# Optimization experiments

Measured on AMD Instinct MI355X. Metric: run time of the kernel, lower is better.

The kernel has to match this reference:

```python
import jax, jax.numpy as jnp
import numpy as np

B, T, C, H = 2, 2048, 1024, 16
D = C // H  # head dim


def setup_inputs() -> dict:
    key = jax.random.key(0)
    k1, k2, k3 = jax.random.split(key, 3)
    x = jax.random.normal(k1, (B, T, C), dtype=jnp.float32)
    w_qkv = jax.random.normal(k2, (3 * C, C), dtype=jnp.float32) * (1.0 / np.sqrt(C))
    b_qkv = jnp.zeros((3 * C,), dtype=jnp.float32)
    w_proj = jax.random.normal(k3, (C, C), dtype=jnp.float32) * (1.0 / np.sqrt(C))
    b_proj = jnp.zeros((C,), dtype=jnp.float32)
    return {"x": x, "w_qkv": w_qkv, "b_qkv": b_qkv, "w_proj": w_proj, "b_proj": b_proj}


def reference(x, w_qkv, b_qkv, w_proj, b_proj):
    # torch Linear: y = x @ W^T + b
    qkv = jnp.einsum('btc,oc->bto', x, w_qkv) + b_qkv  # [B,T,3C]
    q, k, v = jnp.split(qkv, 3, axis=-1)
    # [B,T,C] -> [B,H,T,D]
    reshape = lambda t: t.reshape(B, T, H, D).transpose(0, 2, 1, 3)
    q, k, v = reshape(q), reshape(k), reshape(v)
    scale = 1.0 / jnp.sqrt(jnp.float32(C))  # NOTE: full C, as in source
    att = jnp.einsum('bhtd,bhsd->bhts', q, k) * scale  # [B,H,T,T]
    causal = jnp.tril(jnp.ones((T, T), dtype=bool))
    att = jnp.where(causal, att, -jnp.inf)
    att = jax.nn.softmax(att, axis=-1)
    y = jnp.einsum('bhts,bhsd->bhtd', att, v)  # [B,H,T,D]
    y = y.transpose(0, 2, 1, 3).reshape(B, T, C)
    return jnp.einsum('btc,oc->bto', y, w_proj) + b_proj
```

## Files before the change

### kernel.cpp

```cpp
#include <hip/hip_runtime.h>

#define DEVINL __device__ __forceinline__

typedef __attribute__((ext_vector_type(8))) short short8;
typedef __attribute__((ext_vector_type(4))) float f32x4;

DEVINL unsigned f2bf_u(float x) {
  union { float f; unsigned u; } v; v.f = x;
  unsigned r = v.u + 0x7FFF + ((v.u >> 16) & 1);
  return r >> 16;
}
DEVINL unsigned short f2bf(float x) { return (unsigned short)f2bf_u(x); }

DEVINL unsigned cvt_pk_bf16(float lo, float hi) {
  unsigned r;
  asm("v_cvt_pk_bf16_f32 %0, %1, %2" : "=v"(r) : "v"(lo), "v"(hi));
  return r;
}

DEVINL void permlane32_swap(unsigned& a, unsigned& b) {
  asm volatile("v_permlane32_swap_b32 %0, %1" : "+v"(a), "+v"(b));
}
DEVINL void permlane16_swap(unsigned& a, unsigned& b) {
  asm volatile("v_permlane16_swap_b32 %0, %1" : "+v"(a), "+v"(b));
}

#if __has_builtin(__builtin_amdgcn_exp2f)
#define EXP2(x) __builtin_amdgcn_exp2f(x)
#else
#define EXP2(x) exp2f(x)
#endif

DEVINL void gload_lds16(const void* g, void* l) {
  __builtin_amdgcn_global_load_lds(
      (const __attribute__((address_space(1))) unsigned int*)g,
      (__attribute__((address_space(3))) unsigned int*)l, 16, 0, 0);
}

DEVINL short8 as_s8(uint4 v) { union { uint4 u; short8 s; } c; c.u = v; return c.s; }
DEVINL f32x4 fzero() { f32x4 z = {0.f, 0.f, 0.f, 0.f}; return z; }

__global__ __launch_bounds__(256) void cvt3_kernel(
    const float4* __restrict__ x, const float4* __restrict__ wq,
    const float4* __restrict__ wp, ushort4* __restrict__ xo,
    ushort4* __restrict__ wqo, ushort4* __restrict__ wpo) {
  const int N1 = 1048576, N2 = 1835008, NT = 2097152;
  int i = blockIdx.x * blockDim.x + threadIdx.x;
  int stride = gridDim.x * blockDim.x;
  for (; i < NT; i += stride) {
    const float4* s; ushort4* d; int j;
    if (i < N1) { s = x; d = xo; j = i; }
    else if (i < N2) { s = wq; d = wqo; j = i - N1; }
    else { s = wp; d = wpo; j = i - N2; }
    float4 v = s[j];
    ushort4 o;
    o.x = f2bf(v.x); o.y = f2bf(v.y); o.z = f2bf(v.z); o.w = f2bf(v.w);
    d[j] = o;
  }
}

template <int RX, int RY>
__global__ __launch_bounds__(256, 2) void gemm_qkv(
    const ushort* __restrict__ A, const ushort* __restrict__ Bw,
    const float* __restrict__ bias,
    ushort* __restrict__ Qb, ushort* __restrict__ Kb, ushort* __restrict__ Vt,
    int M, int N, int K) {
  __shared__ __align__(16) char smem[32768];
  char* ldsA = smem;
  char* ldsB = smem + 16384;

  int gx = gridDim.x;
  int id = blockIdx.y * gx + blockIdx.x;
  int xcd = id & 7, slot = id >> 3;
  int rw = gx / RX, rh = gridDim.y / RY;
  int bx = (xcd % RX) * rw + slot % rw;
  int by = (xcd / RX) * rh + slot / rw;

  int m0 = by * 128, n0 = bx * 128;
  int t = threadIdx.x;
  int lane = t & 63, w = t >> 6;
  int q = lane & 15, g = lane >> 4;
  int wr = w >> 1, wc = w & 1;

  int Lrow[4], Lcol[4];
#pragma unroll
  for (int i = 0; i < 4; ++i) {
    int L = i * 4096 + t * 16;
    int row = L >> 7, c = L & 127;
    Lrow[i] = row;
    Lcol[i] = c ^ ((row & 7) << 4);
  }
  const char* Abase = (const char*)A + (size_t)m0 * K * 2;
  const char* Bbase = (const char*)Bw + (size_t)n0 * K * 2;

  f32x4 acc[4][4];
#pragma unroll
  for (int i = 0; i < 4; ++i)
#pragma unroll
    for (int j = 0; j < 4; ++j) acc[i][j] = fzero();

  for (int k0 = 0; k0 < K; k0 += 64) {
    __syncthreads();
#pragma unroll
    for (int i = 0; i < 4; ++i) {
      int L = i * 4096 + t * 16;
      gload_lds16(Abase + (size_t)Lrow[i] * (K * 2) + k0 * 2 + Lcol[i], ldsA + L);
    }
#pragma unroll
    for (int i = 0; i < 4; ++i) {
      int L = i * 4096 + t * 16;
      gload_lds16(Bbase + (size_t)Lrow[i] * (K * 2) + k0 * 2 + Lcol[i], ldsB + L);
    }
    __syncthreads();

    uint4 bf[2][4];
#pragma unroll
    for (int s = 0; s < 2; ++s)
#pragma unroll
      for (int nt = 0; nt < 4; ++nt) {
        int row = wc * 64 + nt * 16 + q;
        int addr = row * 128 + ((g * 16 + 64 * s) ^ ((row & 7) << 4));
        bf[s][nt] = *(const uint4*)(ldsB + addr);
      }
#pragma unroll
    for (int mt = 0; mt < 4; ++mt) {
      int row = wr * 64 + mt * 16 + q;
      int a0 = row * 128 + ((g * 16) ^ ((row & 7) << 4));
      int a1 = row * 128 + ((g * 16 + 64) ^ ((row & 7) << 4));
      uint4 af0 = *(const uint4*)(ldsA + a0);
      uint4 af1 = *(const uint4*)(ldsA + a1);
#pragma unroll
      for (int nt = 0; nt < 4; ++nt) {
        acc[mt][nt] = __builtin_amdgcn_mfma_f32_16x16x32_bf16(
            as_s8(af0), as_s8(bf[0][nt]), acc[mt][nt], 0, 0, 0);
        acc[mt][nt] = __builtin_amdgcn_mfma_f32_16x16x32_bf16(
            as_s8(af1), as_s8(bf[1][nt]), acc[mt][nt], 0, 0, 0);
      }
    }
  }

  int mrow0 = m0 + wr * 64;
  int b = mrow0 >> 11, tt0 = mrow0 & 2047;
  if (n0 >= 2048) {
    int hs = (n0 + wc * 64) >> 6;
    int h = hs & 15;
    ushort* vb = Vt + ((size_t)(b * 16 + h) * 64) * 2048;
#pragma unroll
    for (int nt = 0; nt < 4; ++nt) {
      int d = nt * 16 + q;
      float bv = bias[n0 + wc * 64 + nt * 16 + q];
#pragma unroll
      for (int mt = 0; mt < 4; ++mt) {
        uint2 o;
        o.x = cvt_pk_bf16(acc[mt][nt][0] + bv, acc[mt][nt][1] + bv);
        o.y = cvt_pk_bf16(acc[mt][nt][2] + bv, acc[mt][nt][3] + bv);
        *(uint2*)(vb + (size_t)d * 2048 + tt0 + mt * 16 + g * 4) = o;
      }
    }
  } else {
    __syncthreads();
    char* tile = smem + w * 8192;
    float bv[4];
#pragma unroll
    for (int nt = 0; nt < 4; ++nt) bv[nt] = bias[n0 + wc * 64 + nt * 16 + q];
#pragma unroll
    for (int mt = 0; mt < 4; ++mt)
#pragma unroll
      for (int nt = 0; nt < 4; ++nt)
#pragma unroll
        for (int r = 0; r < 4; ++r) {
          int row = mt * 16 + g * 4 + r;
          int bcol = ((nt * 16 + q) * 2) ^ ((row & 7) << 4);
          *(ushort*)(tile + row * 128 + bcol) = f2bf(acc[mt][nt][r] + bv[nt]);
        }
    int hs = (n0 + wc * 64) >> 6;
    int which = hs >> 4, h = hs & 15;
    ushort* dst = which == 0 ? Qb : Kb;
    ushort* dbase = dst + (size_t)(b * 16 + h) * 131072 + (size_t)tt0 * 64;
#pragma unroll
    for (int p = 0; p < 8; ++p) {
      int row = p * 8 + (lane >> 3);
      int bcol = ((lane & 7) * 16) ^ ((row & 7) << 4);
      uint4 v = *(const uint4*)(tile + row * 128 + bcol);
      *(uint4*)(dbase + (size_t)row * 64 + (lane & 7) * 8) = v;
    }
  }
}

__global__ __launch_bounds__(256, 2) void gemm_proj(
    const ushort* __restrict__ A, const ushort* __restrict__ Bw,
    const float* __restrict__ bias, float* __restrict__ Out,
    int M, int N, int K) {
  __shared__ __align__(16) char smem[24576];

  int gx = gridDim.x;
  int id = blockIdx.y * gx + blockIdx.x;
  int xcd = id & 7, slot = id >> 3;
  int bx = slot & 7;
  int by = xcd * 8 + (slot >> 3);

  int m0 = by * 64, n0 = bx * 128;
  int t = threadIdx.x;
  int lane = t & 63, w = t >> 6;
  int q = lane & 15, g = lane >> 4;
  int wr = w >> 1, wc = w & 1;

  int Lrow[4], Lcol[4];
#pragma unroll
  for (int i = 0; i < 4; ++i) {
    int L = i * 4096 + t * 16;
    int row = L >> 7, c = L & 127;
    Lrow[i] = row;
    Lcol[i] = c ^ ((row & 7) << 4);
  }
  const char* Abase = (const char*)A + (size_t)m0 * K * 2;
  const char* Bbase = (const char*)Bw + (size_t)n0 * K * 2;

  f32x4 acc[2][4];
#pragma unroll
  for (int i = 0; i < 2; ++i)
#pragma unroll
    for (int j = 0; j < 4; ++j) acc[i][j] = fzero();

  for (int k0 = 0; k0 < K; k0 += 64) {
    __syncthreads();
#pragma unroll
    for (int i = 0; i < 2; ++i) {
      int L = i * 4096 + t * 16;
      gload_lds16(Abase + (size_t)Lrow[i] * (K * 2) + k0 * 2 + Lcol[i], smem + L);
    }
#pragma unroll
    for (int i = 0; i < 4; ++i) {
      int L = i * 4096 + t * 16;
      gload_lds16(Bbase + (size_t)Lrow[i] * (K * 2) + k0 * 2 + Lcol[i],
                  smem + 8192 + L);
    }
    __syncthreads();

    uint4 bf[2][4];
#pragma unroll
    for (int s = 0; s < 2; ++s)
#pragma unroll
      for (int nt = 0; nt < 4; ++nt) {
        int row = wc * 64 + nt * 16 + q;
        int addr = 8192 + row * 128 + ((g * 16 + 64 * s) ^ ((row & 7) << 4));
        bf[s][nt] = *(const uint4*)(smem + addr);
      }
    __builtin_amdgcn_s_setprio(1);
#pragma unroll
    for (int mt = 0; mt < 2; ++mt) {
      int row = wr * 32 + mt * 16 + q;
      int a0 = row * 128 + ((g * 16) ^ ((row & 7) << 4));
      int a1 = row * 128 + ((g * 16 + 64) ^ ((row & 7) << 4));
      uint4 af0 = *(const uint4*)(smem + a0);
      uint4 af1 = *(const uint4*)(smem + a1);
#pragma unroll
      for (int nt = 0; nt < 4; ++nt) {
        acc[mt][nt] = __builtin_amdgcn_mfma_f32_16x16x32_bf16(
            as_s8(af0), as_s8(bf[0][nt]), acc[mt][nt], 0, 0, 0);
        acc[mt][nt] = __builtin_amdgcn_mfma_f32_16x16x32_bf16(
            as_s8(af1), as_s8(bf[1][nt]), acc[mt][nt], 0, 0, 0);
      }
    }
    __builtin_amdgcn_s_setprio(0);
  }

#pragma unroll
  for (int nt = 0; nt < 4; ++nt) {
    int ncol = n0 + wc * 64 + nt * 16 + q;
    float bv = bias[ncol];
#pragma unroll
    for (int mt = 0; mt < 2; ++mt)
#pragma unroll
      for (int r = 0; r < 4; ++r) {
        int m = m0 + wr * 32 + mt * 16 + g * 4 + r;
        Out[(size_t)m * N + ncol] = acc[mt][nt][r] + bv;
      }
  }
}

__global__ __launch_bounds__(512) void attn_kernel(
    const ushort* __restrict__ Q, const ushort* __restrict__ K,
    const ushort* __restrict__ Vt, ushort* __restrict__ Y) {
  __shared__ __align__(16) char smem[33280];
  const float C44 = 0.0450842298f;
  int id = blockIdx.x;
  int xcd = id & 7, slot = id >> 3;
  int bh = xcd * 4 + (slot & 3);
  int qt = 31 - (slot >> 2);
  int t = threadIdx.x;
  int lane = t & 63, w = t >> 6;
  int q = lane & 15, g = lane >> 4;
  int wq = w & 3, half = w >> 2;
  int b = bh >> 4, hh = bh & 15;

  const char* Kc0 = (const char*)(K + (size_t)bh * 2048 * 64);
  const char* Vc0 = (const char*)(Vt + (size_t)bh * 64 * 2048);

  int tb = t * 16;
  int srow = tb >> 7;
  int scol = (tb & 127) ^ ((srow & 7) << 4);

  int offK[2][2], offV[4];
#pragma unroll
  for (int sub = 0; sub < 2; ++sub)
#pragma unroll
    for (int s = 0; s < 2; ++s) {
      int row = half * 32 + sub * 16 + q;
      offK[sub][s] = row * 128 + ((g * 16 + 64 * s) ^ ((row & 7) << 4));
    }
#pragma unroll
  for (int ds = 0; ds < 4; ++ds) {
    int row = ds * 16 + q;
    offV[ds] = 8192 + row * 128 + ((half * 64 + g * 16) ^ ((row & 7) << 4));
  }

  int nch = qt + 1;
  int qrow0 = qt * 64 + wq * 16;
  int qg = qrow0 + q;

  uint4 qf[2];
  {
    const ushort* Qrow = Q + ((size_t)bh * 2048 + qrow0 + q) * 64;
    qf[0] = *(const uint4*)(Qrow + g * 8);
    qf[1] = *(const uint4*)(Qrow + 32 + g * 8);
  }

  f32x4 oacc[4];
#pragma unroll
  for (int i = 0; i < 4; ++i) oacc[i] = fzero();
  float l_run = 0.f;

  gload_lds16(Kc0 + (size_t)srow * 128 + scol, smem + tb);
  gload_lds16(Vc0 + (size_t)srow * 4096 + scol, smem + 8192 + tb);
  __syncthreads();

  int cur = 0;
#pragma unroll 1
  for (int c = 0; c < nch; ++c) {
    int kv0 = c * 64;
    if (c + 1 < nch) {
      int kn = kv0 + 64;
      char* dstb = smem + (cur ^ 1) * 16384;
      gload_lds16(Kc0 + (size_t)(kn + srow) * 128 + scol, dstb + tb);
      gload_lds16(Vc0 + (size_t)srow * 4096 + (size_t)kn * 2 + scol,
                  dstb + 8192 + tb);
    }
    const char* base = smem + cur * 16384;
    int kst = kv0 + half * 32;
    if (kst <= qrow0 + 15) {
      f32x4 sacc[2];
      __builtin_amdgcn_s_setprio(1);
#pragma unroll
      for (int sub = 0; sub < 2; ++sub) {
        sacc[sub] = fzero();
#pragma unroll
        for (int s = 0; s < 2; ++s)
          sacc[sub] = __builtin_amdgcn_mfma_f32_16x16x32_bf16(
              as_s8(*(const uint4*)(base + offK[sub][s])), as_s8(qf[s]),
              sacc[sub], 0, 0, 0);
      }
      __builtin_amdgcn_s_setprio(0);

      if (kst + 31 > qrow0) {
#pragma unroll
        for (int sub = 0; sub < 2; ++sub)
#pragma unroll
          for (int r = 0; r < 4; ++r) {
            int kv = kst + sub * 16 + g * 4 + r;
            if (kv > qg) sacc[sub][r] = -3e38f;
          }
      }

      unsigned pk[2][2];
      float psum = 0.f;
#pragma unroll
      for (int sub = 0; sub < 2; ++sub) {
        float p0 = EXP2(sacc[sub][0] * C44);
        float p1 = EXP2(sacc[sub][1] * C44);
        float p2 = EXP2(sacc[sub][2] * C44);
        float p3 = EXP2(sacc[sub][3] * C44);
        psum += (p0 + p1) + (p2 + p3);
        pk[sub][0] = cvt_pk_bf16(p0, p1);
        pk[sub][1] = cvt_pk_bf16(p2, p3);
      }
      l_run += psum;

      unsigned w0 = pk[0][0], w1 = pk[1][0];
      permlane32_swap(w0, w1);
      permlane16_swap(w0, w1);
      unsigned w2 = pk[0][1], w3 = pk[1][1];
      permlane32_swap(w2, w3);
      permlane16_swap(w2, w3);
      uint4 pa; pa.x = w0; pa.y = w2; pa.z = w1; pa.w = w3;

      __builtin_amdgcn_s_setprio(1);
#pragma unroll
      for (int ds = 0; ds < 4; ++ds)
        oacc[ds] = __builtin_amdgcn_mfma_f32_16x16x32_bf16(
            as_s8(pa), as_s8(*(const uint4*)(base + offV[ds])),
            oacc[ds], 0, 0, 0);
      __builtin_amdgcn_s_setprio(0);
    }

    __syncthreads();
    cur ^= 1;
  }

  l_run += __shfl_xor(l_run, 16);
  l_run += __shfl_xor(l_run, 32);
  float* ob = (float*)smem + wq * 1024;
  float* mlb = (float*)(smem + 32768);
  if (half) {
#pragma unroll
    for (int ds = 0; ds < 4; ++ds)
#pragma unroll
      for (int r = 0; r < 4; ++r)
        ob[(g * 4 + r) * 64 + ds * 16 + q] = oacc[ds][r];
    if (g == 0) mlb[wq * 16 + q] = l_run;
  }
  __syncthreads();
  if (!half) {
#pragma unroll
    for (int r = 0; r < 4; ++r) {
      int row = g * 4 + r;
      float lA = __shfl(l_run, row);
      float lB = mlb[wq * 16 + row];
      float linv = 1.0f / (lA + lB);
#pragma unroll
      for (int ds = 0; ds < 4; ++ds) {
        float vB = ob[row * 64 + ds * 16 + q];
        float yv = (oacc[ds][r] + vB) * linv;
        Y[(size_t)(b * 2048 + qrow0 + row) * 1024 + hh * 64 + ds * 16 + q] =
            f2bf(yv);
      }
    }
  }
}

extern "C" void kernel_launch(void* const* d_in, const int* in_sizes, int n_in,
                              void* d_out, int out_size, void* d_ws, size_t ws_size,
                              hipStream_t stream) {
  const float* x = (const float*)d_in[0];
  const float* w_qkv = (const float*)d_in[1];
  const float* b_qkv = (const float*)d_in[2];
  const float* w_proj = (const float*)d_in[3];
  const float* b_proj = (const float*)d_in[4];
  float* out = (float*)d_out;
  char* ws = (char*)d_ws;
  const size_t MB = 1024 * 1024;
  ushort* xb    = (ushort*)(ws + 0 * MB);
  ushort* wqkvb = (ushort*)(ws + 8 * MB);
  ushort* wprojb= (ushort*)(ws + 14 * MB);
  ushort* Qb    = (ushort*)(ws + 16 * MB);
  ushort* Kb    = (ushort*)(ws + 24 * MB);
  ushort* Vt    = (ushort*)(ws + 40 * MB);
  ushort* Yb    = (ushort*)(ws + 48 * MB);

  cvt3_kernel<<<2048, 256, 0, stream>>>((const float4*)x, (const float4*)w_qkv,
                                        (const float4*)w_proj, (ushort4*)xb,
                                        (ushort4*)wqkvb, (ushort4*)wprojb);
  gemm_qkv<2, 4><<<dim3(24, 32), 256, 0, stream>>>(xb, wqkvb, b_qkv, Qb, Kb, Vt,
                                                   4096, 3072, 1024);
  attn_kernel<<<dim3(1024), 512, 0, stream>>>(Qb, Kb, Vt, Yb);
  gemm_proj<<<dim3(8, 64), 256, 0, stream>>>(Yb, wprojb, b_proj, out, 4096,
                                             1024, 1024);
}
```

Before: 89.82 us.

## Double query tile per attention block to reuse K/V fragments across two row groups

Each attention block now handles 128 query rows instead of 64, so each wave processes two 16-row query groups and reuses the K and V fragments it loads from LDS for both. The grid is halved to 512 blocks, and launch bounds now request two blocks per CU. This is meant to cut global and LDS traffic for K/V per unit of work. In exchange it raises register pressure, and the coarser tiles can worsen load balance across the causal triangle.

```diff
diff --git a/kernel.cpp b/kernel.cpp
--- a/kernel.cpp
+++ b/kernel.cpp
@@ -279,7 +279,7 @@
   }
 }
 
-__global__ __launch_bounds__(512) void attn_kernel(
+__global__ __launch_bounds__(512, 2) void attn_kernel(
     const ushort* __restrict__ Q, const ushort* __restrict__ K,
     const ushort* __restrict__ Vt, ushort* __restrict__ Y) {
   __shared__ __align__(16) char smem[33280];
@@ -287,7 +287,7 @@
   int id = blockIdx.x;
   int xcd = id & 7, slot = id >> 3;
   int bh = xcd * 4 + (slot & 3);
-  int qt = 31 - (slot >> 2);
+  int qt = 15 - (slot >> 2);
   int t = threadIdx.x;
   int lane = t & 63, w = t >> 6;
   int q = lane & 15, g = lane >> 4;
@@ -315,21 +315,24 @@
     offV[ds] = 8192 + row * 128 + ((half * 64 + g * 16) ^ ((row & 7) << 4));
   }
 
-  int nch = qt + 1;
-  int qrow0 = qt * 64 + wq * 16;
+  int nch = 2 * qt + 2;
+  int qrow0 = qt * 128 + wq * 32;
   int qg = qrow0 + q;
 
-  uint4 qf[2];
-  {
-    const ushort* Qrow = Q + ((size_t)bh * 2048 + qrow0 + q) * 64;
-    qf[0] = *(const uint4*)(Qrow + g * 8);
-    qf[1] = *(const uint4*)(Qrow + 32 + g * 8);
-  }
-
-  f32x4 oacc[4];
-#pragma unroll
-  for (int i = 0; i < 4; ++i) oacc[i] = fzero();
-  float l_run = 0.f;
+  uint4 qf[2][2];
+#pragma unroll
+  for (int q2 = 0; q2 < 2; ++q2) {
+    const ushort* Qrow = Q + ((size_t)bh * 2048 + qrow0 + q2 * 16 + q) * 64;
+    qf[q2][0] = *(const uint4*)(Qrow + g * 8);
+    qf[q2][1] = *(const uint4*)(Qrow + 32 + g * 8);
+  }
+
+  f32x4 oacc[2][4];
+#pragma unroll
+  for (int q2 = 0; q2 < 2; ++q2)
+#pragma unroll
+    for (int i = 0; i < 4; ++i) oacc[q2][i] = fzero();
+  float l_run[2] = {0.f, 0.f};
 
   gload_lds16(Kc0 + (size_t)srow * 128 + scol, smem + tb);
   gload_lds16(Vc0 + (size_t)srow * 4096 + scol, smem + 8192 + tb);
@@ -348,91 +351,118 @@
     }
     const char* base = smem + cur * 16384;
     int kst = kv0 + half * 32;
-    if (kst <= qrow0 + 15) {
-      f32x4 sacc[2];
-      __builtin_amdgcn_s_setprio(1);
-#pragma unroll
-      for (int sub = 0; sub < 2; ++sub) {
-        sacc[sub] = fzero();
+    if (kst <= qrow0 + 31) {
+      uint4 kf[2][2], vf[4];
+#pragma unroll
+      for (int sub = 0; sub < 2; ++sub)
 #pragma unroll
         for (int s = 0; s < 2; ++s)
-          sacc[sub] = __builtin_amdgcn_mfma_f32_16x16x32_bf16(
-              as_s8(*(const uint4*)(base + offK[sub][s])), as_s8(qf[s]),
-              sacc[sub], 0, 0, 0);
-      }
-      __builtin_amdgcn_s_setprio(0);
-
-      if (kst + 31 > qrow0) {
-#pragma unroll
-        for (int sub = 0; sub < 2; ++sub)
-#pragma unroll
-          for (int r = 0; r < 4; ++r) {
-            int kv = kst + sub * 16 + g * 4 + r;
-            if (kv > qg) sacc[sub][r] = -3e38f;
+          kf[sub][s] = *(const uint4*)(base + offK[sub][s]);
+#pragma unroll
+      for (int ds = 0; ds < 4; ++ds)
+        vf[ds] = *(const uint4*)(base + offV[ds]);
+
+#pragma unroll
+      for (int q2 = 0; q2 < 2; ++q2) {
+        int tbrow = qrow0 + q2 * 16;
+        if (kst <= tbrow + 15) {
+          f32x4 sacc[2];
+          __builtin_amdgcn_s_setprio(1);
+#pragma unroll
+          for (int sub = 0; sub < 2; ++sub) {
+            sacc[sub] = fzero();
+#pragma unroll
+            for (int s = 0; s < 2; ++s)
+              sacc[sub] = __builtin_amdgcn_mfma_f32_16x16x32_bf16(
+                  as_s8(kf[sub][s]), as_s8(qf[q2][s]), sacc[sub], 0, 0, 0);
           }
-      }
-
-      unsigned pk[2][2];
-      float psum = 0.f;
-#pragma unroll
-      for (int sub = 0; sub < 2; ++sub) {
-        float p0 = EXP2(sacc[sub][0] * C44);
-        float p1 = EXP2(sacc[sub][1] * C44);
-        float p2 = EXP2(sacc[sub][2] * C44);
-        float p3 = EXP2(sacc[sub][3] * C44);
-        psum += (p0 + p1) + (p2 + p3);
-        pk[sub][0] = cvt_pk_bf16(p0, p1);
-        pk[sub][1] = cvt_pk_bf16(p2, p3);
-      }
-      l_run += psum;
-
-      unsigned w0 = pk[0][0], w1 = pk[1][0];
-      permlane32_swap(w0, w1);
-      permlane16_swap(w0, w1);
-      unsigned w2 = pk[0][1], w3 = pk[1][1];
-      permlane32_swap(w2, w3);
-      permlane16_swap(w2, w3);
-      uint4 pa; pa.x = w0; pa.y = w2; pa.z = w1; pa.w = w3;
-
-      __builtin_amdgcn_s_setprio(1);
-#pragma unroll
-      for (int ds = 0; ds < 4; ++ds)
-        oacc[ds] = __builtin_amdgcn_mfma_f32_16x16x32_bf16(
-            as_s8(pa), as_s8(*(const uint4*)(base + offV[ds])),
-            oacc[ds], 0, 0, 0);
-      __builtin_amdgcn_s_setprio(0);
+          __builtin_amdgcn_s_setprio(0);
+
+          if (kst + 31 > tbrow) {
+            int qgl = tbrow + q;
+#pragma unroll
+            for (int sub = 0; sub < 2; ++sub)
+#pragma unroll
+              for (int r = 0; r < 4; ++r) {
+                int kv = kst + sub * 16 + g * 4 + r;
+                if (kv > qgl) sacc[sub][r] = -3e38f;
+              }
+          }
+
+          unsigned pk[2][2];
+          float psum = 0.f;
+#pragma unroll
+          for (int sub = 0; sub < 2; ++sub) {
+            float p0 = EXP2(sacc[sub][0] * C44);
+            float p1 = EXP2(sacc[sub][1] * C44);
+            float p2 = EXP2(sacc[sub][2] * C44);
+            float p3 = EXP2(sacc[sub][3] * C44);
+            psum += (p0 + p1) + (p2 + p3);
+            pk[sub][0] = cvt_pk_bf16(p0, p1);
+            pk[sub][1] = cvt_pk_bf16(p2, p3);
+          }
+          l_run[q2] += psum;
+
+          unsigned w0 = pk[0][0], w1 = pk[1][0];
+          permlane32_swap(w0, w1);
+          permlane16_swap(w0, w1);
+          unsigned w2 = pk[0][1], w3 = pk[1][1];
+          permlane32_swap(w2, w3);
+          permlane16_swap(w2, w3);
+          uint4 pa; pa.x = w0; pa.y = w2; pa.z = w1; pa.w = w3;
+
+          __builtin_amdgcn_s_setprio(1);
+#pragma unroll
+          for (int ds = 0; ds < 4; ++ds)
+            oacc[q2][ds] = __builtin_amdgcn_mfma_f32_16x16x32_bf16(
+                as_s8(pa), as_s8(vf[ds]), oacc[q2][ds], 0, 0, 0);
+          __builtin_amdgcn_s_setprio(0);
+        }
+      }
     }
 
     __syncthreads();
     cur ^= 1;
   }
 
-  l_run += __shfl_xor(l_run, 16);
-  l_run += __shfl_xor(l_run, 32);
-  float* ob = (float*)smem + wq * 1024;
+#pragma unroll
+  for (int q2 = 0; q2 < 2; ++q2) {
+    l_run[q2] += __shfl_xor(l_run[q2], 16);
+    l_run[q2] += __shfl_xor(l_run[q2], 32);
+  }
   float* mlb = (float*)(smem + 32768);
   if (half) {
 #pragma unroll
-    for (int ds = 0; ds < 4; ++ds)
-#pragma unroll
-      for (int r = 0; r < 4; ++r)
-        ob[(g * 4 + r) * 64 + ds * 16 + q] = oacc[ds][r];
-    if (g == 0) mlb[wq * 16 + q] = l_run;
+    for (int q2 = 0; q2 < 2; ++q2) {
+      int rb = wq * 2 + q2;
+      float* ob = (float*)smem + rb * 1024;
+#pragma unroll
+      for (int ds = 0; ds < 4; ++ds)
+#pragma unroll
+        for (int r = 0; r < 4; ++r)
+          ob[(g * 4 + r) * 64 + ds * 16 + q] = oacc[q2][ds][r];
+      if (g == 0) mlb[rb * 16 + q] = l_run[q2];
+    }
   }
   __syncthreads();
   if (!half) {
 #pragma unroll
-    for (int r = 0; r < 4; ++r) {
-      int row = g * 4 + r;
-      float lA = __shfl(l_run, row);
-      float lB = mlb[wq * 16 + row];
-      float linv = 1.0f / (lA + lB);
-#pragma unroll
-      for (int ds = 0; ds < 4; ++ds) {
-        float vB = ob[row * 64 + ds * 16 + q];
-        float yv = (oacc[ds][r] + vB) * linv;
-        Y[(size_t)(b * 2048 + qrow0 + row) * 1024 + hh * 64 + ds * 16 + q] =
-            f2bf(yv);
+    for (int q2 = 0; q2 < 2; ++q2) {
+      int rb = wq * 2 + q2;
+      const float* ob = (const float*)smem + rb * 1024;
+#pragma unroll
+      for (int r = 0; r < 4; ++r) {
+        int row = g * 4 + r;
+        float lA = __shfl(l_run[q2], row);
+        float lB = mlb[rb * 16 + row];
+        float linv = 1.0f / (lA + lB);
+#pragma unroll
+        for (int ds = 0; ds < 4; ++ds) {
+          float vB = ob[row * 64 + ds * 16 + q];
+          float yv = (oacc[q2][ds][r] + vB) * linv;
+          Y[(size_t)(b * 2048 + qrow0 + q2 * 16 + row) * 1024 + hh * 64 +
+            ds * 16 + q] = f2bf(yv);
+        }
       }
     }
   }
@@ -462,7 +492,7 @@
                                         (ushort4*)wqkvb, (ushort4*)wprojb);
   gemm_qkv<2, 4><<<dim3(24, 32), 256, 0, stream>>>(xb, wqkvb, b_qkv, Qb, Kb, Vt,
                                                    4096, 3072, 1024);
-  attn_kernel<<<dim3(1024), 512, 0, stream>>>(Qb, Kb, Vt, Yb);
+  attn_kernel<<<dim3(512), 512, 0, stream>>>(Qb, Kb, Vt, Yb);
   gemm_proj<<<dim3(8, 64), 256, 0, stream>>>(Yb, wprojb, b_proj, out, 4096,
                                              1024, 1024);
 }
```

Result: slower. 96.81 us (+7.8%).
